# Performance work log

Hardware: AMD Instinct MI355X
Metric: run time of the kernel (lower is better)

The kernel has to match this reference:

```python
import jax, jax.numpy as jnp
import numpy as np

N = 50000   # nodes
E = 800000  # edges
D = 128     # hidden_dim == input_dim
H = 8       # heads
C = D // H  # per-head dim = 16
ED = 10     # edge_dim
FF = 4 * D  # ffn hidden = 512


def setup_inputs() -> dict:
    key = jax.random.key(0)
    ks = jax.random.split(key, 20)
    s = 0.05
    p = lambda k, shape: (jax.random.normal(k, shape, jnp.float32) * s)
    return {
        "x": jax.random.normal(ks[0], (N, D), jnp.float32),
        "edge_index": jax.random.randint(ks[1], (2, E), 0, N),
        "edge_attr": jax.random.normal(ks[2], (E, ED), jnp.float32),
        # TransformerConv params (PyG): lin_query/key/value have bias, lin_edge no bias,
        # lin_skip has bias, lin_beta no bias
        "Wq": p(ks[3], (D, D)), "bq": jnp.zeros((D,), jnp.float32),
        "Wk": p(ks[4], (D, D)), "bk": jnp.zeros((D,), jnp.float32),
        "Wv": p(ks[5], (D, D)), "bv": jnp.zeros((D,), jnp.float32),
        "We": p(ks[6], (ED, D)),
        "Wskip": p(ks[7], (D, D)), "bskip": jnp.zeros((D,), jnp.float32),
        "Wbeta": p(ks[8], (3 * D, 1)),
        # GraphNorm params
        "gn_w": jnp.ones((D,), jnp.float32),
        "gn_b": jnp.zeros((D,), jnp.float32),
        "gn_ms": jnp.ones((D,), jnp.float32),  # mean_scale
        # FFN params
        "W1": p(ks[9], (D, FF)), "b1": jnp.zeros((FF,), jnp.float32),
        "W2": p(ks[10], (FF, D)), "b2": jnp.zeros((D,), jnp.float32),
    }


def _layer(x, edge_index, edge_attr, Wq, bq, Wk, bk, Wv, bv, We, Wskip, bskip,
           Wbeta, gn_w, gn_b, gn_ms, W1, b1, W2, b2):
    n = x.shape[0]
    src, dst = edge_index[0], edge_index[1]
    # ---- TransformerConv (concat heads, edge-conditioned, beta skip) ----
    q = (x @ Wq + bq).reshape(n, H, C)
    k = (x @ Wk + bk).reshape(n, H, C)
    v = (x @ Wv + bv).reshape(n, H, C)
    e = (edge_attr @ We).reshape(-1, H, C)          # [E,H,C]
    k_j = k[src] + e                                 # gather + edge bias
    alpha = jnp.einsum('ehc,ehc->eh', q[dst], k_j) / jnp.sqrt(jnp.float32(C))
    # segment softmax over incoming edges of each target node
    amax = jax.ops.segment_max(alpha, dst, num_segments=n)      # [N,H]
    ex = jnp.exp(alpha - amax[dst])
    denom = jax.ops.segment_sum(ex, dst, num_segments=n)        # [N,H]
    alpha = ex / (denom[dst] + 1e-16)
    msg = (v[src] + e) * alpha[:, :, None]           # [E,H,C]
    out = jax.ops.segment_sum(msg.reshape(-1, H * C), dst, num_segments=n)  # [N,D]
    # beta-gated root skip
    x_r = x @ Wskip + bskip
    beta = jax.nn.sigmoid(jnp.concatenate([out, x_r, out - x_r], axis=-1) @ Wbeta)
    x_att = beta * x_r + (1.0 - beta) * out
    # ---- residual + GraphNorm (single graph) ----
    h = x + x_att
    mean = h.mean(axis=0)
    hc = h - gn_ms * mean
    var = (hc * hc).mean(axis=0)
    h = hc / jnp.sqrt(var + 1e-5) * gn_w + gn_b
    # ---- FFN with residual (GELU exact, matching torch default) ----
    ffn = jax.nn.gelu(h @ W1 + b1, approximate=False) @ W2 + b2
    return h + ffn


def reference(x, edge_index, edge_attr, Wq, bq, Wk, bk, Wv, bv, We, Wskip,
              bskip, Wbeta, gn_w, gn_b, gn_ms, W1, b1, W2, b2):
    return _layer(x, edge_index, edge_attr, Wq, bq, Wk, bk, Wv, bv, We, Wskip,
                  bskip, Wbeta, gn_w, gn_b, gn_ms, W1, b1, W2, b2)
```

## Files before the change

### kernel.cpp

```cpp
#include <hip/hip_runtime.h>
#include <hip/hip_fp16.h>
#include <math.h>

#define D 128
#define ED 10
#define FF 512
#define TPAD 520
#define XPAD 136

typedef __attribute__((ext_vector_type(4))) float f32x4;
typedef __attribute__((ext_vector_type(8))) short bf16x8;
using h2 = decltype(__builtin_amdgcn_cvt_pkrtz(0.f, 0.f));
typedef __attribute__((ext_vector_type(2))) float f32x2;

__device__ __forceinline__ ushort f2bf(float f) {
  unsigned u = __float_as_uint(f);
  unsigned r = u + 0x7fffu + ((u >> 16) & 1u);
  return (ushort)(r >> 16);
}
__device__ __forceinline__ float bf2f(ushort u) {
  return __uint_as_float(((unsigned)u) << 16);
}

#if __has_builtin(__builtin_amdgcn_cvt_pk_f32_fp8) && __has_builtin(__builtin_amdgcn_cvt_pk_fp8_f32)
#define FP8_HW 1
#else
#define FP8_HW 0
#endif

__device__ __forceinline__ unsigned sw_f2fp8(float f) {
  unsigned u = __float_as_uint(f);
  unsigned s = (u >> 24) & 0x80;
  int e = (int)((u >> 23) & 0xff) - 127;
  unsigned mant = u & 0x7fffff;
  if (e < -9) return s;
  if (e > 8) return s | 0x7e;
  if (e >= -6) {
    unsigned m = mant + 0x7ffff + ((mant >> 20) & 1);
    if (m >= 0x800000) { m = 0; ++e; if (e > 8) return s | 0x7e; }
    return s | ((unsigned)(e + 7) << 3) | (m >> 20);
  }
  unsigned full = 0x800000 | mant;
  int shift = 20 + (-6 - e);
  unsigned m = (full + (1u << (shift - 1)) + ((full >> shift) & 1)) >> shift;
  if (m >= 8) return s | 0x08;
  return s | m;
}
__device__ __forceinline__ float sw_fp82f(unsigned b) {
  unsigned s = (b & 0x80) << 24;
  unsigned e = (b >> 3) & 0xf;
  unsigned m = b & 7;
  if (e == 0) {
    if (m == 0) return __uint_as_float(s);
    float v = (float)(int)m * 0.001953125f;
    return (b & 0x80) ? -v : v;
  }
  return __uint_as_float(s | ((e + 120) << 23) | (m << 20));
}

__device__ __forceinline__ ushort pack_fp8_pair(float a, float b) {
#if FP8_HW
  int r = __builtin_amdgcn_cvt_pk_fp8_f32(a, b, 0, false);
  return (ushort)(r & 0xffff);
#else
  return (ushort)(sw_f2fp8(a) | (sw_f2fp8(b) << 8));
#endif
}
template <bool HI>
__device__ __forceinline__ f32x2 unpack_fp8_pair(unsigned w) {
#if FP8_HW
  auto r = __builtin_amdgcn_cvt_pk_f32_fp8((int)w, HI);
  f32x2 o; o[0] = r[0]; o[1] = r[1];
  return o;
#else
  unsigned v = HI ? (w >> 16) : w;
  f32x2 o; o[0] = sw_fp82f(v & 0xff); o[1] = sw_fp82f((v >> 8) & 0xff);
  return o;
#endif
}

__global__ void prep_hist(const float* __restrict__ Wq, const float* __restrict__ Wk,
                          const float* __restrict__ Wv, const float* __restrict__ Wskip,
                          const float* __restrict__ bq, const float* __restrict__ bk,
                          const float* __restrict__ bv, const float* __restrict__ bskip,
                          const float* __restrict__ W1, const float* __restrict__ W2,
                          const int* __restrict__ dst, int* __restrict__ deg,
                          int* __restrict__ rank, int E,
                          ushort* __restrict__ Wcat_t, float* __restrict__ bcat,
                          ushort* __restrict__ W1t, ushort* __restrict__ W2t) {
  int b = blockIdx.x;
  if (b >= 256) {
    int t = (b - 256) * 256 + threadIdx.x;
    if (t < E) rank[t] = atomicAdd(&deg[dst[t]], 1);
    return;
  }
  int t = b * 256 + threadIdx.x;
  {
    int w = t >> 14, c = (t >> 7) & 127, kk = t & 127;
    const float* W = (w == 0) ? Wq : (w == 1) ? Wk : (w == 2) ? Wv : Wskip;
    Wcat_t[t] = f2bf(W[kk * D + c]);
  }
  {
    int f = t >> 7, kk = t & 127;
    W1t[t] = f2bf(W1[kk * FF + f]);
  }
  {
    int c = t >> 9, f = t & 511;
    W2t[t] = f2bf(W2[f * D + c]);
  }
  if (t < 4 * D) {
    int w = t >> 7;
    const float* bb = (w == 0) ? bq : (w == 1) ? bk : (w == 2) ? bv : bskip;
    bcat[t] = bb[t & 127];
  }
}

__global__ __launch_bounds__(1024) void scan_kernel(const int* __restrict__ deg,
                                                    int* __restrict__ off, int n) {
  __shared__ int part[1024];
  int t = threadIdx.x;
  int chunk = (n + 1023) / 1024;
  int lo = t * chunk, hi = min(lo + chunk, n);
  int s = 0;
  for (int i = lo; i < hi; ++i) s += deg[i];
  part[t] = s;
  __syncthreads();
  for (int dd = 1; dd < 1024; dd <<= 1) {
    int v = (t >= dd) ? part[t - dd] : 0;
    __syncthreads();
    part[t] += v;
    __syncthreads();
  }
  int excl = (t == 0) ? 0 : part[t - 1];
  for (int i = lo; i < hi; ++i) {
    off[i] = excl;
    excl += deg[i];
  }
  if (t == 1023) off[n] = part[1023];
}

__global__ void scatter_kernel(const int* __restrict__ dst, const int* __restrict__ src,
                               const int* __restrict__ rank, const int* __restrict__ off,
                               const float* __restrict__ attr, int* __restrict__ srcs,
                               unsigned* __restrict__ attrh, int E) {
  int t = blockIdx.x * blockDim.x + threadIdx.x;
  if (t >= E) return;
  int pos = off[dst[t]] + rank[t];
  srcs[pos] = src[t];
  const float2* ap = reinterpret_cast<const float2*>(attr + (size_t)t * ED);
#pragma unroll
  for (int j = 0; j < 5; ++j) {
    float2 av = ap[j];
    h2 hh = __builtin_amdgcn_cvt_pkrtz(av.x, av.y);
    attrh[(size_t)pos * 5 + j] = __builtin_bit_cast(unsigned, hh);
  }
}

__global__ __launch_bounds__(256) void gemm_in(
    const float* __restrict__ x, const ushort* __restrict__ Wcat_t,
    const float* __restrict__ bcat, ushort* __restrict__ qb, unsigned* __restrict__ kvf8,
    float* __restrict__ xr, int n) {
  __shared__ ushort xa[32 * XPAD];
  int r0 = blockIdx.x * 32;
  {
    int row = threadIdx.x >> 3;
    int seg = threadIdx.x & 7;
    int grow = min(r0 + row, n - 1);
    const float4* p = reinterpret_cast<const float4*>(x + (size_t)grow * D + seg * 16);
    float4 f0 = p[0], f1 = p[1], f2 = p[2], f3 = p[3];
    bf16x8 u0, u1;
    u0[0] = (short)f2bf(f0.x); u0[1] = (short)f2bf(f0.y);
    u0[2] = (short)f2bf(f0.z); u0[3] = (short)f2bf(f0.w);
    u0[4] = (short)f2bf(f1.x); u0[5] = (short)f2bf(f1.y);
    u0[6] = (short)f2bf(f1.z); u0[7] = (short)f2bf(f1.w);
    u1[0] = (short)f2bf(f2.x); u1[1] = (short)f2bf(f2.y);
    u1[2] = (short)f2bf(f2.z); u1[3] = (short)f2bf(f2.w);
    u1[4] = (short)f2bf(f3.x); u1[5] = (short)f2bf(f3.y);
    u1[6] = (short)f2bf(f3.z); u1[7] = (short)f2bf(f3.w);
    ushort* dl = xa + row * XPAD + seg * 16;
    *reinterpret_cast<bf16x8*>(dl) = u0;
    *reinterpret_cast<bf16x8*>(dl + 8) = u1;
  }
  __syncthreads();
  int wv = threadIdx.x >> 6;
  int l = threadIdx.x & 63;
  int lr = l & 15, lg = l >> 4;
  const ushort* Wt = Wcat_t + wv * D * D;
  f32x4 acc[2][8];
#pragma unroll
  for (int m = 0; m < 2; ++m)
#pragma unroll
    for (int nn = 0; nn < 8; ++nn) acc[m][nn] = (f32x4)0.f;
#pragma unroll
  for (int kb2 = 0; kb2 < 4; ++kb2) {
    int k0 = kb2 * 32 + lg * 8;
    bf16x8 a[2];
#pragma unroll
    for (int m = 0; m < 2; ++m)
      a[m] = *reinterpret_cast<const bf16x8*>(xa + (m * 16 + lr) * XPAD + k0);
    bf16x8 b[8];
#pragma unroll
    for (int nn = 0; nn < 8; ++nn)
      b[nn] = *reinterpret_cast<const bf16x8*>(Wt + (nn * 16 + lr) * D + k0);
#pragma unroll
    for (int m = 0; m < 2; ++m)
#pragma unroll
      for (int nn = 0; nn < 8; ++nn)
        acc[m][nn] = __builtin_amdgcn_mfma_f32_16x16x32_bf16(a[m], b[nn], acc[m][nn], 0, 0, 0);
  }
#pragma unroll
  for (int m = 0; m < 2; ++m)
#pragma unroll
    for (int nn = 0; nn < 8; ++nn) {
      int col = nn * 16 + lr;
      float bb = bcat[wv * D + col];
#pragma unroll
      for (int j = 0; j < 4; ++j) {
        int row = r0 + m * 16 + lg * 4 + j;
        float val = acc[m][nn][j] + bb;
        if (wv == 1 || wv == 2) {
          float partner = __shfl_xor(val, 1, 64);
          if (((lr & 1) == 0) && row < n) {
            ushort us = pack_fp8_pair(val, partner);
            size_t idx = ((size_t)row * 64 + nn * 8 + (lr >> 1)) * 2 + (wv - 1);
            reinterpret_cast<ushort*>(kvf8)[idx] = us;
          }
        } else if (row < n) {
          if (wv == 0) qb[(size_t)row * D + col] = f2bf(val);
          else xr[(size_t)row * D + col] = val;
        }
      }
    }
}

__global__ __launch_bounds__(256) void node_attn(
    const int* __restrict__ srcs, const int* __restrict__ off,
    const unsigned* __restrict__ attrh, const float* __restrict__ We,
    const ushort* __restrict__ qb, const unsigned* __restrict__ kvf8,
    const float* __restrict__ xr, const float* __restrict__ x,
    const float* __restrict__ Wbeta, float* __restrict__ h,
    float* __restrict__ sums, int n) {
  __shared__ unsigned attrS[4][64][5];
  __shared__ float rs_h[4 * D], rs_h2[4 * D];
  int wid = threadIdx.x >> 6;
  int l = threadIdx.x & 63;
  int d0 = 2 * l;
  h2 wA[5], wB[5];
#pragma unroll
  for (int t = 0; t < 5; ++t) {
    wA[t] = __builtin_amdgcn_cvt_pkrtz(We[(2 * t) * D + d0], We[(2 * t + 1) * D + d0]);
    wB[t] = __builtin_amdgcn_cvt_pkrtz(We[(2 * t) * D + d0 + 1], We[(2 * t + 1) * D + d0 + 1]);
  }
  float2 wb0 = *reinterpret_cast<const float2*>(Wbeta + d0);
  float2 wb1 = *reinterpret_cast<const float2*>(Wbeta + D + d0);
  float2 wb2 = *reinterpret_cast<const float2*>(Wbeta + 2 * D + d0);
  float s_h0 = 0.f, s_h20 = 0.f, s_h1 = 0.f, s_h21 = 0.f;
  for (int node = blockIdx.x * 4 + wid; node < n; node += gridDim.x * 4) {
    const ushort2 qu = *reinterpret_cast<const ushort2*>(qb + (size_t)node * D + d0);
    float q0 = bf2f(qu.x) * 0.25f, q1 = bf2f(qu.y) * 0.25f;
    int o0 = off[node], dg = off[node + 1] - o0;
    float m = -1e30f, den = 0.f, acc0 = 0.f, acc1 = 0.f;
    for (int chunk = 0; chunk < dg; chunk += 64) {
      int cnt = min(64, dg - chunk);
      int s_l = 0;
      if (l < cnt) {
        size_t pos = (size_t)(o0 + chunk + l);
        s_l = srcs[pos];
        const unsigned* ah = attrh + pos * 5;
#pragma unroll
        for (int j = 0; j < 5; ++j) attrS[wid][l][j] = ah[j];
      }
      auto LD = [&](int idx) -> unsigned {
        int ss = __shfl(s_l, min(idx, cnt - 1));
        return kvf8[(size_t)ss * 64 + l];
      };
      auto PROC = [&](unsigned kvw, int i) {
        h2 a0 = __builtin_bit_cast(h2, attrS[wid][i][0]);
        h2 a1 = __builtin_bit_cast(h2, attrS[wid][i][1]);
        h2 a2 = __builtin_bit_cast(h2, attrS[wid][i][2]);
        h2 a3 = __builtin_bit_cast(h2, attrS[wid][i][3]);
        h2 a4 = __builtin_bit_cast(h2, attrS[wid][i][4]);
        float ec0 = __builtin_amdgcn_fdot2(a0, wA[0], 0.f, false);
        ec0 = __builtin_amdgcn_fdot2(a1, wA[1], ec0, false);
        ec0 = __builtin_amdgcn_fdot2(a2, wA[2], ec0, false);
        ec0 = __builtin_amdgcn_fdot2(a3, wA[3], ec0, false);
        ec0 = __builtin_amdgcn_fdot2(a4, wA[4], ec0, false);
        float ec1 = __builtin_amdgcn_fdot2(a0, wB[0], 0.f, false);
        ec1 = __builtin_amdgcn_fdot2(a1, wB[1], ec1, false);
        ec1 = __builtin_amdgcn_fdot2(a2, wB[2], ec1, false);
        ec1 = __builtin_amdgcn_fdot2(a3, wB[3], ec1, false);
        ec1 = __builtin_amdgcn_fdot2(a4, wB[4], ec1, false);
        f32x2 kf = unpack_fp8_pair<false>(kvw);
        f32x2 vf = unpack_fp8_pair<true>(kvw);
        float kk0 = kf[0] + ec0, kk1 = kf[1] + ec1;
        float vv0 = vf[0] + ec0, vv1 = vf[1] + ec1;
        float p = fmaf(q0, kk0, q1 * kk1);
        p += __shfl_xor(p, 1, 8);
        p += __shfl_xor(p, 2, 8);
        p += __shfl_xor(p, 4, 8);
        if (__any(p > m + 8.f)) {
          float mn = fmaxf(m, p);
          float sc = __expf(m - mn);
          den *= sc; acc0 *= sc; acc1 *= sc;
          m = mn;
        }
        float ex = __expf(p - m);
        den += ex;
        acc0 = fmaf(ex, vv0, acc0);
        acc1 = fmaf(ex, vv1, acc1);
      };
      unsigned p0 = LD(0), p1 = LD(1), p2 = LD(2), p3 = LD(3),
               p4 = LD(4), p5 = LD(5), p6 = LD(6), p7 = LD(7);
      for (int i = 0; i < cnt; i += 8) {
        unsigned c0 = p0, c1 = p1, c2 = p2, c3 = p3, c4 = p4, c5 = p5, c6 = p6, c7 = p7;
        p0 = LD(i + 8);  p1 = LD(i + 9);  p2 = LD(i + 10); p3 = LD(i + 11);
        p4 = LD(i + 12); p5 = LD(i + 13); p6 = LD(i + 14); p7 = LD(i + 15);
        PROC(c0, i);
        if (i + 1 < cnt) PROC(c1, i + 1);
        if (i + 2 < cnt) PROC(c2, i + 2);
        if (i + 3 < cnt) PROC(c3, i + 3);
        if (i + 4 < cnt) PROC(c4, i + 4);
        if (i + 5 < cnt) PROC(c5, i + 5);
        if (i + 6 < cnt) PROC(c6, i + 6);
        if (i + 7 < cnt) PROC(c7, i + 7);
      }
    }
    float inv = 1.f / (den + 1e-16f);
    float oo0 = acc0 * inv, oo1 = acc1 * inv;
    float2 xr2 = *reinterpret_cast<const float2*>(xr + (size_t)node * D + d0);
    float2 x2 = *reinterpret_cast<const float2*>(x + (size_t)node * D + d0);
    float pb = oo0 * wb0.x + xr2.x * wb1.x + (oo0 - xr2.x) * wb2.x
             + oo1 * wb0.y + xr2.y * wb1.y + (oo1 - xr2.y) * wb2.y;
#pragma unroll
    for (int msk = 1; msk < 64; msk <<= 1) pb += __shfl_xor(pb, msk, 64);
    float beta = 1.f / (1.f + __expf(-pb));
    float h0 = x2.x + beta * xr2.x + (1.f - beta) * oo0;
    float h1 = x2.y + beta * xr2.y + (1.f - beta) * oo1;
    *reinterpret_cast<float2*>(h + (size_t)node * D + d0) = make_float2(h0, h1);
    s_h0 += h0; s_h20 += h0 * h0;
    s_h1 += h1; s_h21 += h1 * h1;
  }
  rs_h[wid * D + d0] = s_h0;   rs_h[wid * D + d0 + 1] = s_h1;
  rs_h2[wid * D + d0] = s_h20; rs_h2[wid * D + d0 + 1] = s_h21;
  __syncthreads();
  if (threadIdx.x < D) {
    int d = threadIdx.x;
    float sh = rs_h[d] + rs_h[D + d] + rs_h[2 * D + d] + rs_h[3 * D + d];
    float sh2 = rs_h2[d] + rs_h2[D + d] + rs_h2[2 * D + d] + rs_h2[3 * D + d];
    atomicAdd(&sums[d], sh);
    atomicAdd(&sums[D + d], sh2);
  }
}

__global__ __launch_bounds__(256) void ffn_fused(
    const float* __restrict__ h, const float* __restrict__ sums,
    const float* __restrict__ gn_w, const float* __restrict__ gn_b,
    const float* __restrict__ gn_ms,
    const ushort* __restrict__ W1t, const float* __restrict__ b1,
    const ushort* __restrict__ W2t, const float* __restrict__ b2,
    float* __restrict__ out, float inv_n, int n) {
  __shared__ ushort xa[32 * XPAD];
  __shared__ ushort tt[32 * TPAD];
  __shared__ float scsh[2 * D];
  if (threadIdx.x < D) {
    int d = threadIdx.x;
    float mean = sums[d] * inv_n;
    float ex2 = sums[D + d] * inv_n;
    float ms = gn_ms[d];
    float var = ex2 - 2.f * ms * mean * mean + ms * ms * mean * mean;
    float inv = 1.f / sqrtf(var + 1e-5f);
    float scale = gn_w[d] * inv;
    scsh[d] = scale;
    scsh[D + d] = gn_b[d] - ms * mean * scale;
  }
  __syncthreads();
  int r0 = blockIdx.x * 32;
  {
    int row = threadIdx.x >> 3;
    int seg = threadIdx.x & 7;
    int grow = min(r0 + row, n - 1);
    const float4* p = reinterpret_cast<const float4*>(h + (size_t)grow * D + seg * 16);
    float4 f0 = p[0], f1 = p[1], f2 = p[2], f3 = p[3];
    const float4* sc = reinterpret_cast<const float4*>(scsh + seg * 16);
    const float4* sh = reinterpret_cast<const float4*>(scsh + D + seg * 16);
    float4 s0 = sc[0], s1 = sc[1], s2 = sc[2], s3 = sc[3];
    float4 t0 = sh[0], t1 = sh[1], t2 = sh[2], t3 = sh[3];
    bf16x8 u0, u1;
    u0[0] = (short)f2bf(f0.x * s0.x + t0.x); u0[1] = (short)f2bf(f0.y * s0.y + t0.y);
    u0[2] = (short)f2bf(f0.z * s0.z + t0.z); u0[3] = (short)f2bf(f0.w * s0.w + t0.w);
    u0[4] = (short)f2bf(f1.x * s1.x + t1.x); u0[5] = (short)f2bf(f1.y * s1.y + t1.y);
    u0[6] = (short)f2bf(f1.z * s1.z + t1.z); u0[7] = (short)f2bf(f1.w * s1.w + t1.w);
    u1[0] = (short)f2bf(f2.x * s2.x + t2.x); u1[1] = (short)f2bf(f2.y * s2.y + t2.y);
    u1[2] = (short)f2bf(f2.z * s2.z + t2.z); u1[3] = (short)f2bf(f2.w * s2.w + t2.w);
    u1[4] = (short)f2bf(f3.x * s3.x + t3.x); u1[5] = (short)f2bf(f3.y * s3.y + t3.y);
    u1[6] = (short)f2bf(f3.z * s3.z + t3.z); u1[7] = (short)f2bf(f3.w * s3.w + t3.w);
    ushort* dl = xa + row * XPAD + seg * 16;
    *reinterpret_cast<bf16x8*>(dl) = u0;
    *reinterpret_cast<bf16x8*>(dl + 8) = u1;
  }
  __syncthreads();
  int wv = threadIdx.x >> 6;
  int l = threadIdx.x & 63;
  int lr = l & 15, lg = l >> 4;
  int c0 = wv * 128;
  {
    f32x4 acc[2][8];
#pragma unroll
    for (int m = 0; m < 2; ++m)
#pragma unroll
      for (int nn = 0; nn < 8; ++nn) acc[m][nn] = (f32x4)0.f;
#pragma unroll
    for (int kb = 0; kb < 4; ++kb) {
      int k0 = kb * 32 + lg * 8;
      bf16x8 a[2];
#pragma unroll
      for (int m = 0; m < 2; ++m)
        a[m] = *reinterpret_cast<const bf16x8*>(xa + (m * 16 + lr) * XPAD + k0);
      bf16x8 b[8];
#pragma unroll
      for (int nn = 0; nn < 8; ++nn)
        b[nn] = *reinterpret_cast<const bf16x8*>(W1t + (c0 + nn * 16 + lr) * D + k0);
#pragma unroll
      for (int m = 0; m < 2; ++m)
#pragma unroll
        for (int nn = 0; nn < 8; ++nn)
          acc[m][nn] = __builtin_amdgcn_mfma_f32_16x16x32_bf16(a[m], b[nn], acc[m][nn], 0, 0, 0);
    }
    const float inv_sqrt2 = 0.70710678118654752440f;
#pragma unroll
    for (int m = 0; m < 2; ++m)
#pragma unroll
      for (int nn = 0; nn < 8; ++nn) {
        int col = c0 + nn * 16 + lr;
        float bb = b1[col];
#pragma unroll
        for (int j = 0; j < 4; ++j) {
          int rowl = m * 16 + lg * 4 + j;
          float val = acc[m][nn][j] + bb;
          val = 0.5f * val * (1.f + erff(val * inv_sqrt2));
          tt[rowl * TPAD + col] = f2bf(val);
        }
      }
  }
  __syncthreads();
  {
    f32x4 acc[2][2];
#pragma unroll
    for (int m = 0; m < 2; ++m)
#pragma unroll
      for (int nn = 0; nn < 2; ++nn) acc[m][nn] = (f32x4)0.f;
#pragma unroll 4
    for (int kb = 0; kb < 16; ++kb) {
      int k0 = kb * 32 + lg * 8;
      bf16x8 a[2];
#pragma unroll
      for (int m = 0; m < 2; ++m)
        a[m] = *reinterpret_cast<const bf16x8*>(tt + (m * 16 + lr) * TPAD + k0);
      bf16x8 b[2];
#pragma unroll
      for (int nn = 0; nn < 2; ++nn)
        b[nn] = *reinterpret_cast<const bf16x8*>(W2t + (wv * 32 + nn * 16 + lr) * FF + k0);
#pragma unroll
      for (int m = 0; m < 2; ++m)
#pragma unroll
        for (int nn = 0; nn < 2; ++nn)
          acc[m][nn] = __builtin_amdgcn_mfma_f32_16x16x32_bf16(a[m], b[nn], acc[m][nn], 0, 0, 0);
    }
#pragma unroll
    for (int m = 0; m < 2; ++m)
#pragma unroll
      for (int nn = 0; nn < 2; ++nn) {
        int col = wv * 32 + nn * 16 + lr;
        float bb = b2[col];
#pragma unroll
        for (int j = 0; j < 4; ++j) {
          int rowl = m * 16 + lg * 4 + j;
          int row = r0 + rowl;
          if (row < n) {
            float hn = bf2f(xa[rowl * XPAD + col]);
            out[(size_t)row * D + col] = hn + acc[m][nn][j] + bb;
          }
        }
      }
  }
}

extern "C" void kernel_launch(void* const* d_in, const int* in_sizes, int n_in,
                              void* d_out, int out_size, void* d_ws, size_t ws_size,
                              hipStream_t stream) {
  const float* x     = (const float*)d_in[0];
  const int*   ei    = (const int*)d_in[1];
  const float* attr  = (const float*)d_in[2];
  const float* Wq    = (const float*)d_in[3];
  const float* bq    = (const float*)d_in[4];
  const float* Wk    = (const float*)d_in[5];
  const float* bk    = (const float*)d_in[6];
  const float* Wv    = (const float*)d_in[7];
  const float* bv    = (const float*)d_in[8];
  const float* We    = (const float*)d_in[9];
  const float* Wskip = (const float*)d_in[10];
  const float* bskip = (const float*)d_in[11];
  const float* Wbeta = (const float*)d_in[12];
  const float* gn_w  = (const float*)d_in[13];
  const float* gn_b  = (const float*)d_in[14];
  const float* gn_ms = (const float*)d_in[15];
  const float* W1    = (const float*)d_in[16];
  const float* b1    = (const float*)d_in[17];
  const float* W2    = (const float*)d_in[18];
  const float* b2    = (const float*)d_in[19];

  const int n = in_sizes[0] / D;
  const int E = in_sizes[1] / 2;
  const int* src = ei;
  const int* dst = ei + E;
  const size_t ND = (size_t)n * D;

  ushort* qb = (ushort*)d_ws;
  unsigned* kvf8 = (unsigned*)(qb + ND);
  float* xr = (float*)(kvf8 + (size_t)n * 64);
  int* deg = (int*)(xr + ND);
  float* sums = (float*)(deg + n);
  int* off = (int*)(sums + 2 * D);
  int* srcs = off + n + 1;
  int* rank = srcs + E;
  unsigned* attrh = (unsigned*)(rank + E);
  ushort* Wcat_t = (ushort*)(attrh + (size_t)E * 5);
  ushort* W1t = Wcat_t + 4 * D * D;
  ushort* W2t = W1t + D * FF;
  float* bcat = (float*)(W2t + FF * D);

  (void)hipMemsetAsync(deg, 0, ((size_t)n + 2 * D) * sizeof(int), stream);

  int ghist = (E + 255) / 256;
  prep_hist<<<256 + ghist, 256, 0, stream>>>(Wq, Wk, Wv, Wskip, bq, bk, bv, bskip, W1, W2,
                                             dst, deg, rank, E, Wcat_t, bcat, W1t, W2t);
  scan_kernel<<<1, 1024, 0, stream>>>(deg, off, n);
  scatter_kernel<<<ghist, 256, 0, stream>>>(dst, src, rank, off, attr, srcs, attrh, E);

  gemm_in<<<(n + 31) / 32, 256, 0, stream>>>(x, Wcat_t, bcat, qb, kvf8, xr, n);

  node_attn<<<2048, 256, 0, stream>>>(srcs, off, attrh, We, qb, kvf8, xr, x, Wbeta,
                                      (float*)d_out, sums, n);

  ffn_fused<<<(n + 31) / 32, 256, 0, stream>>>((const float*)d_out, sums, gn_w, gn_b, gn_ms,
                                               W1t, b1, W2t, b2, (float*)d_out,
                                               1.f / (float)n, n);
}
```

Before: 416.2 us.

## Merge edge scatter into input GEMM and streamline attention inner loop

The edge scatter kernel is folded into the input projection GEMM as extra blocks of one launch. That removes a kernel boundary and lets the memory-bound scatter overlap with the GEMM blocks. In node_attn, the per-edge attribute staging in LDS moves from a 5-word stride to a uint4 plus a separate word, so reads are vectorized. The load is made branch-free by clamping the edge position, and the shuffle index is simplified. The first two butterfly reduction steps use DPP quad permutes instead of ds_swizzle/bpermute shuffles.

New measurement: 385.6 us. -7.4%, faster.

```diff
diff --git a/kernel.cpp b/kernel.cpp
--- a/kernel.cpp
+++ b/kernel.cpp
@@ -20,6 +20,15 @@
 }
 __device__ __forceinline__ float bf2f(ushort u) {
   return __uint_as_float(((unsigned)u) << 16);
+}
+
+__device__ __forceinline__ float dpp_add_xor1(float x) {
+  int y = __builtin_amdgcn_update_dpp(0, __builtin_bit_cast(int, x), 0xB1, 0xF, 0xF, true);
+  return x + __builtin_bit_cast(float, y);
+}
+__device__ __forceinline__ float dpp_add_xor2(float x) {
+  int y = __builtin_amdgcn_update_dpp(0, __builtin_bit_cast(int, x), 0x4E, 0xF, 0xF, true);
+  return x + __builtin_bit_cast(float, y);
 }
 
 #if __has_builtin(__builtin_amdgcn_cvt_pk_f32_fp8) && __has_builtin(__builtin_amdgcn_cvt_pk_fp8_f32)
@@ -139,27 +148,28 @@
   if (t == 1023) off[n] = part[1023];
 }
 
-__global__ void scatter_kernel(const int* __restrict__ dst, const int* __restrict__ src,
-                               const int* __restrict__ rank, const int* __restrict__ off,
-                               const float* __restrict__ attr, int* __restrict__ srcs,
-                               unsigned* __restrict__ attrh, int E) {
-  int t = blockIdx.x * blockDim.x + threadIdx.x;
-  if (t >= E) return;
-  int pos = off[dst[t]] + rank[t];
-  srcs[pos] = src[t];
-  const float2* ap = reinterpret_cast<const float2*>(attr + (size_t)t * ED);
-#pragma unroll
-  for (int j = 0; j < 5; ++j) {
-    float2 av = ap[j];
-    h2 hh = __builtin_amdgcn_cvt_pkrtz(av.x, av.y);
-    attrh[(size_t)pos * 5 + j] = __builtin_bit_cast(unsigned, hh);
-  }
-}
-
-__global__ __launch_bounds__(256) void gemm_in(
+__global__ __launch_bounds__(256) void gemm_scatter(
     const float* __restrict__ x, const ushort* __restrict__ Wcat_t,
     const float* __restrict__ bcat, ushort* __restrict__ qb, unsigned* __restrict__ kvf8,
-    float* __restrict__ xr, int n) {
+    float* __restrict__ xr, int n, int gm,
+    const int* __restrict__ dst, const int* __restrict__ src, const int* __restrict__ rank,
+    const int* __restrict__ off, const float* __restrict__ attr, int* __restrict__ srcs,
+    unsigned* __restrict__ attrh, int E) {
+  if ((int)blockIdx.x >= gm) {
+    int t = ((int)blockIdx.x - gm) * 256 + threadIdx.x;
+    if (t < E) {
+      int pos = off[dst[t]] + rank[t];
+      srcs[pos] = src[t];
+      const float2* ap = reinterpret_cast<const float2*>(attr + (size_t)t * ED);
+#pragma unroll
+      for (int j = 0; j < 5; ++j) {
+        float2 av = ap[j];
+        h2 hh = __builtin_amdgcn_cvt_pkrtz(av.x, av.y);
+        attrh[(size_t)pos * 5 + j] = __builtin_bit_cast(unsigned, hh);
+      }
+    }
+    return;
+  }
   __shared__ ushort xa[32 * XPAD];
   int r0 = blockIdx.x * 32;
   {
@@ -240,7 +250,8 @@
     const float* __restrict__ xr, const float* __restrict__ x,
     const float* __restrict__ Wbeta, float* __restrict__ h,
     float* __restrict__ sums, int n) {
-  __shared__ unsigned attrS[4][64][5];
+  __shared__ uint4 attrS4[4][64];
+  __shared__ unsigned attrS1[4][64];
   __shared__ float rs_h[4 * D], rs_h2[4 * D];
   int wid = threadIdx.x >> 6;
   int l = threadIdx.x & 63;
@@ -262,24 +273,27 @@
     float m = -1e30f, den = 0.f, acc0 = 0.f, acc1 = 0.f;
     for (int chunk = 0; chunk < dg; chunk += 64) {
       int cnt = min(64, dg - chunk);
-      int s_l = 0;
-      if (l < cnt) {
-        size_t pos = (size_t)(o0 + chunk + l);
-        s_l = srcs[pos];
-        const unsigned* ah = attrh + pos * 5;
-#pragma unroll
-        for (int j = 0; j < 5; ++j) attrS[wid][l][j] = ah[j];
+      long pos = (long)o0 + chunk + l;
+      long pend = (long)o0 + dg - 1;
+      if (pos > pend) pos = pend;
+      int s_l = srcs[pos];
+      {
+        const unsigned* ah = attrh + (size_t)pos * 5;
+        attrS4[wid][l] = make_uint4(ah[0], ah[1], ah[2], ah[3]);
+        attrS1[wid][l] = ah[4];
       }
       auto LD = [&](int idx) -> unsigned {
-        int ss = __shfl(s_l, min(idx, cnt - 1));
+        int ss = __shfl(s_l, idx & 63, 64);
         return kvf8[(size_t)ss * 64 + l];
       };
       auto PROC = [&](unsigned kvw, int i) {
-        h2 a0 = __builtin_bit_cast(h2, attrS[wid][i][0]);
-        h2 a1 = __builtin_bit_cast(h2, attrS[wid][i][1]);
-        h2 a2 = __builtin_bit_cast(h2, attrS[wid][i][2]);
-        h2 a3 = __builtin_bit_cast(h2, attrS[wid][i][3]);
-        h2 a4 = __builtin_bit_cast(h2, attrS[wid][i][4]);
+        uint4 av = attrS4[wid][i];
+        unsigned av1 = attrS1[wid][i];
+        h2 a0 = __builtin_bit_cast(h2, av.x);
+        h2 a1 = __builtin_bit_cast(h2, av.y);
+        h2 a2 = __builtin_bit_cast(h2, av.z);
+        h2 a3 = __builtin_bit_cast(h2, av.w);
+        h2 a4 = __builtin_bit_cast(h2, av1);
         float ec0 = __builtin_amdgcn_fdot2(a0, wA[0], 0.f, false);
         ec0 = __builtin_amdgcn_fdot2(a1, wA[1], ec0, false);
         ec0 = __builtin_amdgcn_fdot2(a2, wA[2], ec0, false);
@@ -295,8 +309,8 @@
         float kk0 = kf[0] + ec0, kk1 = kf[1] + ec1;
         float vv0 = vf[0] + ec0, vv1 = vf[1] + ec1;
         float p = fmaf(q0, kk0, q1 * kk1);
-        p += __shfl_xor(p, 1, 8);
-        p += __shfl_xor(p, 2, 8);
+        p = dpp_add_xor1(p);
+        p = dpp_add_xor2(p);
         p += __shfl_xor(p, 4, 8);
         if (__any(p > m + 8.f)) {
           float mn = fmaxf(m, p);
@@ -535,9 +549,10 @@
   prep_hist<<<256 + ghist, 256, 0, stream>>>(Wq, Wk, Wv, Wskip, bq, bk, bv, bskip, W1, W2,
                                              dst, deg, rank, E, Wcat_t, bcat, W1t, W2t);
   scan_kernel<<<1, 1024, 0, stream>>>(deg, off, n);
-  scatter_kernel<<<ghist, 256, 0, stream>>>(dst, src, rank, off, attr, srcs, attrh, E);
-
-  gemm_in<<<(n + 31) / 32, 256, 0, stream>>>(x, Wcat_t, bcat, qb, kvf8, xr, n);
+
+  int gm = (n + 31) / 32;
+  gemm_scatter<<<gm + ghist, 256, 0, stream>>>(x, Wcat_t, bcat, qb, kvf8, xr, n, gm, dst,
+                                               src, rank, off, attr, srcs, attrh, E);
 
   node_attn<<<2048, 256, 0, stream>>>(srcs, off, attrh, We, qb, kvf8, xr, x, Wbeta,
                                       (float*)d_out, sums, n);
```
